# Kernel tuning notes

Measured on AMD Instinct MI355X. Metric: run time of the kernel, lower is better.

## Reference

```python
import jax, jax.numpy as jnp
import numpy as np

SPATIAL_SHAPES = ((64, 64), (32, 32), (16, 16), (8, 8))  # (H_l, W_l) per level
N_HEADS, N_LEVELS, N_POINTS = 8, 4, 4
EMBED, HEAD_DIM = 256, 32


def _bilinear_sample(v_lvl, loc, H, W):
    """grid_sample(mode=bilinear, padding=zeros, align_corners=False).

    v_lvl: (B, nH, H*W, d)   loc: (B, Nq, nH, P, 2) with (x, y) in [0, 1].
    Returns (B, nH, Nq, P, d).
    """
    B, nH, _, d = v_lvl.shape
    Nq, P = loc.shape[1], loc.shape[3]
    g = 2.0 * loc - 1.0                      # normalized [-1, 1]
    px = ((g[..., 0] + 1.0) * W - 1.0) * 0.5  # pixel coords, align_corners=False
    py = ((g[..., 1] + 1.0) * H - 1.0) * 0.5
    x0 = jnp.floor(px); y0 = jnp.floor(py)
    wx = px - x0; wy = py - y0
    x0i = x0.astype(jnp.int32); y0i = y0.astype(jnp.int32)
    acc = jnp.zeros((B, nH, Nq * P, d), v_lvl.dtype)
    corners = ((0, 0, (1 - wx) * (1 - wy)), (1, 0, wx * (1 - wy)),
               (0, 1, (1 - wx) * wy), (1, 1, wx * wy))
    for dx, dy, w in corners:
        xi = x0i + dx; yi = y0i + dy
        valid = (xi >= 0) & (xi < W) & (yi >= 0) & (yi < H)
        idx = jnp.clip(yi, 0, H - 1) * W + jnp.clip(xi, 0, W - 1)  # (B,Nq,nH,P)
        idx_t = idx.transpose(0, 2, 1, 3).reshape(B, nH, Nq * P)
        wm = jnp.where(valid, w, 0.0).astype(v_lvl.dtype)
        wm = wm.transpose(0, 2, 1, 3).reshape(B, nH, Nq * P, 1)
        gathered = jnp.take_along_axis(v_lvl, idx_t[..., None], axis=2)
        acc = acc + wm * gathered
    return acc.reshape(B, nH, Nq, P, d)


def setup_inputs() -> dict:
    key = jax.random.key(0)
    ks = jax.random.split(key, 12)
    B, Nq = 4, sum(H * W for H, W in SPATIAL_SHAPES)
    Nv = Nq
    s = 1.0 / np.sqrt(EMBED)
    return {
        "query": jax.random.normal(ks[0], (B, Nq, EMBED), jnp.float32),
        "value": jax.random.normal(ks[1], (B, Nv, EMBED), jnp.float32),
        "reference_points": jax.random.uniform(ks[2], (B, Nq, N_LEVELS, 2), jnp.float32),
        "value_proj_w": jax.random.normal(ks[3], (EMBED, EMBED), jnp.float32) * s,
        "value_proj_b": jnp.zeros((EMBED,), jnp.float32),
        "offsets_w": jax.random.normal(ks[4], (EMBED, N_HEADS * N_LEVELS * N_POINTS * 2), jnp.float32) * (0.05 * s),
        "offsets_b": jax.random.normal(ks[5], (N_HEADS * N_LEVELS * N_POINTS * 2,), jnp.float32) * 2.0,
        "attn_w_w": jax.random.normal(ks[6], (EMBED, N_HEADS * N_LEVELS * N_POINTS), jnp.float32) * s,
        "attn_w_b": jnp.zeros((N_HEADS * N_LEVELS * N_POINTS,), jnp.float32),
        "out_w": jax.random.normal(ks[7], (EMBED, EMBED), jnp.float32) * s,
        "out_b": jnp.zeros((EMBED,), jnp.float32),
    }


def reference(query, value, reference_points, value_proj_w, value_proj_b,
              offsets_w, offsets_b, attn_w_w, attn_w_b, out_w, out_b):
    B, Nq, C = query.shape
    Nv = value.shape[1]
    v = (value @ value_proj_w + value_proj_b).reshape(B, Nv, N_HEADS, HEAD_DIM)
    off = (query @ offsets_w + offsets_b).reshape(B, Nq, N_HEADS, N_LEVELS, N_POINTS, 2)
    aw = (query @ attn_w_w + attn_w_b).reshape(B, Nq, N_HEADS, N_LEVELS * N_POINTS)
    aw = jax.nn.softmax(aw, axis=-1).reshape(B, Nq, N_HEADS, N_LEVELS, N_POINTS)
    norm = jnp.array([[W, H] for H, W in SPATIAL_SHAPES], dtype=query.dtype)  # (L,2) as (W,H)
    loc = reference_points[:, :, None, :, None, :] + off / norm[None, None, None, :, None, :]
    out = jnp.zeros((B, Nq, N_HEADS, HEAD_DIM), query.dtype)
    cursor = 0
    for l, (H, W) in enumerate(SPATIAL_SHAPES):
        v_lvl = v[:, cursor:cursor + H * W].transpose(0, 2, 1, 3)  # (B,nH,HW,d)
        cursor += H * W
        sampled = _bilinear_sample(v_lvl, loc[:, :, :, l], H, W)   # (B,nH,Nq,P,d)
        out = out + jnp.einsum('bnhp,bhnpd->bnhd', aw[:, :, :, l], sampled)
    return out.reshape(B, Nq, C) @ out_w + out_b
```

## Files before the change

kernel.cpp:

```cpp
#include <hip/hip_runtime.h>
#include <hip/hip_bf16.h>
#include <math.h>

#define B_ 4
#define NQ 5440
#define M_ROWS (B_ * NQ)
#define NH 8
#define NL 4
#define NP 4
#define HD 32

typedef __attribute__((ext_vector_type(8))) short bf16x8;
typedef __attribute__((ext_vector_type(4))) short bf16x4;
typedef __attribute__((ext_vector_type(4))) float f32x4;
typedef _Float16 f16;

static __device__ __forceinline__ unsigned short f2bf(float f) {
  union { float f; unsigned u; } v; v.f = f;
  unsigned r = (v.u + 0x7fffu + ((v.u >> 16) & 1u)) >> 16;
  return (unsigned short)r;
}
static __device__ __forceinline__ float bits2f(unsigned u) {
  union { unsigned u; float f; } v; v.u = u; return v.f;
}

__global__ __launch_bounds__(256) void prep_all(
    const float* __restrict__ value, const float* __restrict__ query,
    unsigned short* __restrict__ value_bf, unsigned short* __restrict__ query_bf,
    const float* __restrict__ vpw, const float* __restrict__ offw,
    const float* __restrict__ attnw, const float* __restrict__ outw,
    const float* __restrict__ offb, const float* __restrict__ attnb,
    unsigned short* __restrict__ vp_t, unsigned short* __restrict__ q_t,
    unsigned short* __restrict__ out_t, float* __restrict__ biasq, int n4) {
  int id = blockIdx.x * 256 + threadIdx.x;
  if (id < 2 * n4) {
    const float* src; unsigned short* dst; int j;
    if (id < n4) { src = value; dst = value_bf; j = id; }
    else { src = query; dst = query_bf; j = id - n4; }
    float4 f = ((const float4*)src)[j];
    bf16x4 o;
    o[0] = (short)f2bf(f.x); o[1] = (short)f2bf(f.y);
    o[2] = (short)f2bf(f.z); o[3] = (short)f2bf(f.w);
    ((bf16x4*)dst)[j] = o;
    return;
  }
  int w = id - 2 * n4;
  if (w < 65536) {
    int n = w >> 8, k = w & 255;
    vp_t[w] = f2bf(vpw[k * 256 + n]);
  } else if (w < 163840) {
    int q = w - 65536; int n = q >> 8, k = q & 255;
    q_t[q] = f2bf(n < 256 ? offw[k * 256 + n] : attnw[k * 128 + (n - 256)]);
  } else if (w < 229376) {
    int o = w - 163840; int n = o >> 8, k = o & 255;
    out_t[o] = f2bf(outw[k * 256 + n]);
  } else if (w < 229760) {
    int j = w - 229376;
    biasq[j] = j < 256 ? offb[j] : attnb[j - 256];
  }
}

__global__ __launch_bounds__(256) void gemm12_kernel(
    const unsigned short* __restrict__ valbf, const unsigned short* __restrict__ qrybf,
    const unsigned short* __restrict__ wt_vp, const unsigned short* __restrict__ wt_q,
    const float* __restrict__ vp_b, const float* __restrict__ biasq,
    unsigned short* __restrict__ v_bf, f16* __restrict__ offaw_h) {
  __shared__ unsigned short Bs[8 * 64 * 32];
  const int t = threadIdx.x;
  const int lane = t & 63, wid = t >> 6;
  const int qd = lane >> 4, l16 = lane & 15;
  const int g = blockIdx.x;
  const int grp = g / 80, r = g % 80;
  int by, bx;
  if (grp < 21) { by = grp * 8 + (r & 7); bx = r >> 3; }
  else          { by = 168 + (r & 1);     bx = r >> 1; }
  const int bm = by * 128;
  const bool isv = bx < 4;
  const int bn = isv ? bx * 64 : (bx - 4) * 64;
  const unsigned short* A  = isv ? valbf : qrybf;
  const unsigned short* Wt = isv ? wt_vp : wt_q;

  const unsigned short* bg = Wt + (size_t)(bn + (t >> 2)) * 256 + (t & 3) * 8;
  unsigned short* bs_b = Bs + (t & 192) * 8;
#pragma unroll
  for (int j = 0; j < 8; ++j)
    __builtin_amdgcn_global_load_lds(
        (const __attribute__((address_space(1))) void*)(bg + j * 32),
        (__attribute__((address_space(3))) void*)(bs_b + j * 2048), 16, 0, 0);

  const unsigned short* ar0 = A + (size_t)(bm + wid * 32 + l16) * 256 + qd * 8;
  const unsigned short* ar1 = ar0 + 16 * 256;
  __syncthreads();

  f32x4 acc[2][4] = {};
#pragma unroll
  for (int j = 0; j < 8; ++j) {
    const bf16x8 af0 = *(const bf16x8*)(ar0 + j * 32);
    const bf16x8 af1 = *(const bf16x8*)(ar1 + j * 32);
    const unsigned short* bt = Bs + j * 2048 + l16 * 32 + qd * 8;
#pragma unroll
    for (int ni = 0; ni < 4; ++ni) {
      const bf16x8 bf = *(const bf16x8*)(bt + ni * 512);
      acc[0][ni] = __builtin_amdgcn_mfma_f32_16x16x32_bf16(af0, bf, acc[0][ni], 0, 0, 0);
      acc[1][ni] = __builtin_amdgcn_mfma_f32_16x16x32_bf16(af1, bf, acc[1][ni], 0, 0, 0);
    }
  }
  if (isv) {
#pragma unroll
    for (int ni = 0; ni < 4; ++ni) {
      const int c = bn + ni * 16 + l16;
      const float bb = vp_b[c];
      const int h = c >> 5, d = c & 31;
#pragma unroll
      for (int mi = 0; mi < 2; ++mi)
#pragma unroll
        for (int rr = 0; rr < 4; ++rr) {
          const int gm = bm + wid * 32 + mi * 16 + qd * 4 + rr;
          const int b = gm / NQ, pix = gm - b * NQ;
          v_bf[((size_t)(b * NH + h) * NQ + pix) * HD + d] = f2bf(acc[mi][ni][rr] + bb);
        }
    }
  } else {
#pragma unroll
    for (int ni = 0; ni < 4; ++ni) {
      const int c = bn + ni * 16 + l16;
      const float bb = biasq[c];
#pragma unroll
      for (int mi = 0; mi < 2; ++mi)
#pragma unroll
        for (int rr = 0; rr < 4; ++rr) {
          const int gm = bm + wid * 32 + mi * 16 + qd * 4 + rr;
          offaw_h[(size_t)gm * 384 + c] = (f16)(acc[mi][ni][rr] + bb);
        }
    }
  }
}

__global__ __launch_bounds__(256) void gemm_out_kernel(
    const unsigned short* __restrict__ attn_bf, const unsigned short* __restrict__ wt_out,
    const float* __restrict__ out_b, float* __restrict__ out) {
  __shared__ unsigned short Bs[8 * 64 * 32];
  const int t = threadIdx.x;
  const int lane = t & 63, wid = t >> 6;
  const int qd = lane >> 4, l16 = lane & 15;
  const int g = blockIdx.x;
  const int grp = g / 32, r = g % 32;
  int by, bx;
  if (grp < 21) { by = grp * 8 + (r & 7); bx = r >> 3; }
  else          { by = 168 + (r & 1);     bx = r >> 1; }
  const int bm = by * 128, bn = bx * 64;

  const unsigned short* bg = wt_out + (size_t)(bn + (t >> 2)) * 256 + (t & 3) * 8;
  unsigned short* bs_b = Bs + (t & 192) * 8;
#pragma unroll
  for (int j = 0; j < 8; ++j)
    __builtin_amdgcn_global_load_lds(
        (const __attribute__((address_space(1))) void*)(bg + j * 32),
        (__attribute__((address_space(3))) void*)(bs_b + j * 2048), 16, 0, 0);

  const unsigned short* ar0 = attn_bf + (size_t)(bm + wid * 32 + l16) * 256 + qd * 8;
  const unsigned short* ar1 = ar0 + 16 * 256;
  __syncthreads();

  f32x4 acc[2][4] = {};
#pragma unroll
  for (int j = 0; j < 8; ++j) {
    const bf16x8 af0 = *(const bf16x8*)(ar0 + j * 32);
    const bf16x8 af1 = *(const bf16x8*)(ar1 + j * 32);
    const unsigned short* bt = Bs + j * 2048 + l16 * 32 + qd * 8;
#pragma unroll
    for (int ni = 0; ni < 4; ++ni) {
      const bf16x8 bf = *(const bf16x8*)(bt + ni * 512);
      acc[0][ni] = __builtin_amdgcn_mfma_f32_16x16x32_bf16(af0, bf, acc[0][ni], 0, 0, 0);
      acc[1][ni] = __builtin_amdgcn_mfma_f32_16x16x32_bf16(af1, bf, acc[1][ni], 0, 0, 0);
    }
  }
#pragma unroll
  for (int ni = 0; ni < 4; ++ni) {
    const int c = bn + ni * 16 + l16;
    const float bb = out_b[c];
#pragma unroll
    for (int mi = 0; mi < 2; ++mi)
#pragma unroll
      for (int rr = 0; rr < 4; ++rr) {
        const int gm = bm + wid * 32 + mi * 16 + qd * 4 + rr;
        out[(size_t)gm * 256 + c] = acc[mi][ni][rr] + bb;
      }
  }
}

__global__ __launch_bounds__(256) void sample_fused_kernel(
    const unsigned short* __restrict__ v, const float* __restrict__ refp,
    const f16* __restrict__ offaw_h, unsigned short* __restrict__ out) {
  __shared__ float s_off[8 * 384];
  __shared__ float s_ref[64];
  __shared__ unsigned s_offs[16 * 64 * 4];
  __shared__ float s_wts[16 * 64 * 4];
  const int t = threadIdx.x;
  const int blk = blockIdx.x;
  const int b = (blk & 7) >> 1;
  const int q0loc = ((blk >> 3) * 2 + (blk & 1)) * 8;
  const int q0 = b * NQ + q0loc;

  {
    const unsigned* src = (const unsigned*)(offaw_h + (size_t)q0 * 384);
#pragma unroll
    for (int i = 0; i < 6; ++i) {
      const int idx = t + i * 256;
      union { unsigned u; f16 h[2]; } cv; cv.u = src[idx];
      s_off[2 * idx]     = (float)cv.h[0];
      s_off[2 * idx + 1] = (float)cv.h[1];
    }
    if (t < 64) s_ref[t] = refp[(size_t)q0 * 8 + t];
  }
  __syncthreads();
  if (t < 64) {
    float* p = s_off + (t >> 3) * 384 + 256 + (t & 7) * 16;
    float m = -1e30f;
#pragma unroll
    for (int j = 0; j < 16; ++j) m = fmaxf(m, p[j]);
    float e[16]; float s = 0.f;
#pragma unroll
    for (int j = 0; j < 16; ++j) { e[j] = __expf(p[j] - m); s += e[j]; }
    const float inv = 1.f / s;
#pragma unroll
    for (int j = 0; j < 16; ++j) p[j] = e[j] * inv;
  }
  __syncthreads();
  {
    const int qh = t & 63, q = qh >> 3, h = qh & 7, l = t >> 6;
    const int HS[NL]      = {64, 32, 16, 8};
    const int LVL_OFF[NL] = {0, 4096, 5120, 5376};
    const int H = HS[l], W = HS[l];
    const float rx = s_ref[q * 8 + l * 2 + 0];
    const float ry = s_ref[q * 8 + l * 2 + 1];
    const unsigned vbase = (unsigned)(((b * NH + h) * NQ + LVL_OFF[l]) * 64);
#pragma unroll
    for (int pp = 0; pp < 4; ++pp) {
      const int p = l * 4 + pp;
      const float ox = s_off[q * 384 + h * 32 + l * 8 + pp * 2 + 0];
      const float oy = s_off[q * 384 + h * 32 + l * 8 + pp * 2 + 1];
      const float a  = s_off[q * 384 + 256 + h * 16 + p];
      const float px = rx * (float)W + ox - 0.5f;
      const float py = ry * (float)H + oy - 0.5f;
      const float x0f = floorf(px), y0f = floorf(py);
      const int x0 = (int)x0f, y0 = (int)y0f;
      const int x1 = x0 + 1, y1 = y0 + 1;
      const float wx = px - x0f, wy = py - y0f;
      const float m_x0 = (x0 >= 0 && x0 < W) ? 1.f : 0.f;
      const float m_x1 = (x1 >= 0 && x1 < W) ? 1.f : 0.f;
      const float m_y0 = (y0 >= 0 && y0 < H) ? 1.f : 0.f;
      const float m_y1 = (y1 >= 0 && y1 < H) ? 1.f : 0.f;
      const int cx0 = min(max(x0, 0), W - 1), cx1 = min(max(x1, 0), W - 1);
      const int cy0 = min(max(y0, 0), H - 1), cy1 = min(max(y1, 0), H - 1);
      const int ti = (p * 64 + qh) * 4;
      uint4 o4;
      o4.x = vbase + (unsigned)((cy0 * W + cx0) * 64);
      o4.y = vbase + (unsigned)((cy0 * W + cx1) * 64);
      o4.z = vbase + (unsigned)((cy1 * W + cx0) * 64);
      o4.w = vbase + (unsigned)((cy1 * W + cx1) * 64);
      float4 w4;
      w4.x = a * (1.f - wx) * (1.f - wy) * m_x0 * m_y0;
      w4.y = a * wx * (1.f - wy) * m_x1 * m_y0;
      w4.z = a * (1.f - wx) * wy * m_x0 * m_y1;
      w4.w = a * wx * wy * m_x1 * m_y1;
      *(uint4*)&s_offs[ti] = o4;
      *(float4*)&s_wts[ti] = w4;
    }
  }
  __syncthreads();
  const int lane = t & 63, wave = t >> 6;
  const int qloc = wave * 2 + (lane >> 5);
  const int h = (lane >> 2) & 7, d8 = lane & 3;
  const int tqh = qloc * 8 + h;
  const char* vB = (const char*)v;
  const int dof = d8 * 16;
  float acc[8] = {};
#pragma unroll 4
  for (int p = 0; p < 16; ++p) {
    const uint4  o4 = *(const uint4*)&s_offs[(p * 64 + tqh) * 4];
    const float4 w4 = *(const float4*)&s_wts[(p * 64 + tqh) * 4];
    const unsigned off[4] = {o4.x, o4.y, o4.z, o4.w};
    const float wt[4] = {w4.x, w4.y, w4.z, w4.w};
#pragma unroll
    for (int c = 0; c < 4; ++c) {
      union { bf16x8 v8; unsigned u[4]; } cc;
      cc.v8 = *(const bf16x8*)(vB + off[c] + dof);
      const float w = wt[c];
#pragma unroll
      for (int k = 0; k < 4; ++k) {
        acc[2 * k]     += w * bits2f(cc.u[k] << 16);
        acc[2 * k + 1] += w * bits2f(cc.u[k] & 0xffff0000u);
      }
    }
  }
  const int bq = q0 + qloc;
  bf16x8 ov;
#pragma unroll
  for (int k = 0; k < 8; ++k) ov[k] = (short)f2bf(acc[k]);
  *(bf16x8*)(out + (size_t)bq * 256 + h * HD + d8 * 8) = ov;
}

extern "C" void kernel_launch(void* const* d_in, const int* in_sizes, int n_in,
                              void* d_out, int out_size, void* d_ws, size_t ws_size,
                              hipStream_t stream) {
  const float* query        = (const float*)d_in[0];
  const float* value        = (const float*)d_in[1];
  const float* refp         = (const float*)d_in[2];
  const float* value_proj_w = (const float*)d_in[3];
  const float* value_proj_b = (const float*)d_in[4];
  const float* offsets_w    = (const float*)d_in[5];
  const float* offsets_b    = (const float*)d_in[6];
  const float* attn_w_w     = (const float*)d_in[7];
  const float* attn_w_b     = (const float*)d_in[8];
  const float* out_w        = (const float*)d_in[9];
  const float* out_b        = (const float*)d_in[10];
  float* out = (float*)d_out;

  const int M = M_ROWS;
  const size_t SZ_V   = (size_t)M * 256 * 2;
  const size_t SZ_OFF = (size_t)M * 384 * 2;
  char* w = (char*)d_ws;
  unsigned short* value_bf = (unsigned short*)w;
  unsigned short* attn_bf  = (unsigned short*)w;
  unsigned short* query_bf = (unsigned short*)(w + SZ_V);
  unsigned short* v_bf     = (unsigned short*)(w + 2 * SZ_V);
  f16* offaw_h             = (f16*)(w + 3 * SZ_V);
  char* wts                = w + 3 * SZ_V + SZ_OFF;
  unsigned short* wt_vp    = (unsigned short*)wts;
  unsigned short* wt_q     = wt_vp + 65536;
  unsigned short* wt_out   = wt_q + 98304;
  float* biasq             = (float*)(wt_out + 65536);

  dim3 blk(256);
  const int n4 = M * 64;
  const int prep_blocks = (2 * n4 + 229760 + 255) / 256;
  prep_all<<<prep_blocks, blk, 0, stream>>>(
      value, query, value_bf, query_bf,
      value_proj_w, offsets_w, attn_w_w, out_w, offsets_b, attn_w_b,
      wt_vp, wt_q, wt_out, biasq, n4);
  gemm12_kernel<<<1700, blk, 0, stream>>>(
      value_bf, query_bf, wt_vp, wt_q, value_proj_b, biasq, v_bf, offaw_h);
  sample_fused_kernel<<<M / 8, blk, 0, stream>>>(v_bf, refp, offaw_h, attn_bf);
  gemm_out_kernel<<<680, blk, 0, stream>>>(attn_bf, wt_out, out_b, out);
}
```

Measured before the change: 174.1 us.

## Shrink sampler LDS with padded aliased layout, fp16 weights, packed FMA

The sampling kernel's shared memory is rearranged. Offsets and attention logits go into padded rows to avoid bank conflicts, and the per-tap offset table aliases the same buffer after values are pulled into registers behind an extra barrier. Bilinear corner weights are stored as fp16 instead of fp32, and accumulation uses two-wide float vectors so the compiler can emit packed FMA. The aim is a much smaller LDS footprint for higher occupancy and fewer ALU instructions in the gather loop, at the cost of an extra sync and reduced weight precision.

Result: slower. 184.5 us (+5.9%).

```diff
diff --git a/kernel.cpp b/kernel.cpp
--- a/kernel.cpp
+++ b/kernel.cpp
@@ -13,7 +13,9 @@
 typedef __attribute__((ext_vector_type(8))) short bf16x8;
 typedef __attribute__((ext_vector_type(4))) short bf16x4;
 typedef __attribute__((ext_vector_type(4))) float f32x4;
+typedef __attribute__((ext_vector_type(2))) float f32x2;
 typedef _Float16 f16;
+typedef __attribute__((ext_vector_type(4))) _Float16 f16x4;
 
 static __device__ __forceinline__ unsigned short f2bf(float f) {
   union { float f; unsigned u; } v; v.f = f;
@@ -192,10 +194,13 @@
 __global__ __launch_bounds__(256) void sample_fused_kernel(
     const unsigned short* __restrict__ v, const float* __restrict__ refp,
     const f16* __restrict__ offaw_h, unsigned short* __restrict__ out) {
-  __shared__ float s_off[8 * 384];
-  __shared__ float s_ref[64];
-  __shared__ unsigned s_offs[16 * 64 * 4];
-  __shared__ float s_wts[16 * 64 * 4];
+  __shared__ __align__(16) char smem[24832];
+  float*    s_offp = (float*)smem;
+  float*    s_aw   = (float*)(smem + 8448);
+  unsigned* s_toff = (unsigned*)smem;
+  f16*      s_twt  = (f16*)(smem + 16384);
+  float*    s_ref  = (float*)(smem + 24576);
+
   const int t = threadIdx.x;
   const int blk = blockIdx.x;
   const int b = (blk & 7) >> 1;
@@ -207,15 +212,24 @@
 #pragma unroll
     for (int i = 0; i < 6; ++i) {
       const int idx = t + i * 256;
+      const int q = idx / 192, u = idx - q * 192;
       union { unsigned u; f16 h[2]; } cv; cv.u = src[idx];
-      s_off[2 * idx]     = (float)cv.h[0];
-      s_off[2 * idx + 1] = (float)cv.h[1];
+      const float lo = (float)cv.h[0], hi = (float)cv.h[1];
+      const int c = 2 * u;
+      if (c < 256) {
+        float* d = s_offp + (q * 8 + (c >> 5)) * 33 + (c & 31);
+        d[0] = lo; d[1] = hi;
+      } else {
+        const int cc = c - 256;
+        float* d = s_aw + (q * 8 + (cc >> 4)) * 17 + (cc & 15);
+        d[0] = lo; d[1] = hi;
+      }
     }
     if (t < 64) s_ref[t] = refp[(size_t)q0 * 8 + t];
   }
   __syncthreads();
   if (t < 64) {
-    float* p = s_off + (t >> 3) * 384 + 256 + (t & 7) * 16;
+    float* p = s_aw + t * 17;
     float m = -1e30f;
 #pragma unroll
     for (int j = 0; j < 16; ++j) m = fmaxf(m, p[j]);
@@ -227,20 +241,27 @@
     for (int j = 0; j < 16; ++j) p[j] = e[j] * inv;
   }
   __syncthreads();
+  const int qh = t & 63, l = t >> 6;
+  const int q = qh >> 3, h = qh & 7;
+  float offv[8], awv[4];
+#pragma unroll
+  for (int i = 0; i < 8; ++i) offv[i] = s_offp[qh * 33 + l * 8 + i];
+#pragma unroll
+  for (int i = 0; i < 4; ++i) awv[i] = s_aw[qh * 17 + l * 4 + i];
+  const float rx = s_ref[q * 8 + l * 2 + 0];
+  const float ry = s_ref[q * 8 + l * 2 + 1];
+  __syncthreads();
   {
-    const int qh = t & 63, q = qh >> 3, h = qh & 7, l = t >> 6;
     const int HS[NL]      = {64, 32, 16, 8};
     const int LVL_OFF[NL] = {0, 4096, 5120, 5376};
     const int H = HS[l], W = HS[l];
-    const float rx = s_ref[q * 8 + l * 2 + 0];
-    const float ry = s_ref[q * 8 + l * 2 + 1];
     const unsigned vbase = (unsigned)(((b * NH + h) * NQ + LVL_OFF[l]) * 64);
 #pragma unroll
     for (int pp = 0; pp < 4; ++pp) {
       const int p = l * 4 + pp;
-      const float ox = s_off[q * 384 + h * 32 + l * 8 + pp * 2 + 0];
-      const float oy = s_off[q * 384 + h * 32 + l * 8 + pp * 2 + 1];
-      const float a  = s_off[q * 384 + 256 + h * 16 + p];
+      const float ox = offv[pp * 2 + 0];
+      const float oy = offv[pp * 2 + 1];
+      const float a  = awv[pp];
       const float px = rx * (float)W + ox - 0.5f;
       const float py = ry * (float)H + oy - 0.5f;
       const float x0f = floorf(px), y0f = floorf(py);
@@ -259,46 +280,49 @@
       o4.y = vbase + (unsigned)((cy0 * W + cx1) * 64);
       o4.z = vbase + (unsigned)((cy1 * W + cx0) * 64);
       o4.w = vbase + (unsigned)((cy1 * W + cx1) * 64);
-      float4 w4;
-      w4.x = a * (1.f - wx) * (1.f - wy) * m_x0 * m_y0;
-      w4.y = a * wx * (1.f - wy) * m_x1 * m_y0;
-      w4.z = a * (1.f - wx) * wy * m_x0 * m_y1;
-      w4.w = a * wx * wy * m_x1 * m_y1;
-      *(uint4*)&s_offs[ti] = o4;
-      *(float4*)&s_wts[ti] = w4;
+      f16x4 w4;
+      w4[0] = (f16)(a * (1.f - wx) * (1.f - wy) * m_x0 * m_y0);
+      w4[1] = (f16)(a * wx * (1.f - wy) * m_x1 * m_y0);
+      w4[2] = (f16)(a * (1.f - wx) * wy * m_x0 * m_y1);
+      w4[3] = (f16)(a * wx * wy * m_x1 * m_y1);
+      *(uint4*)&s_toff[ti] = o4;
+      *(f16x4*)&s_twt[ti] = w4;
     }
   }
   __syncthreads();
   const int lane = t & 63, wave = t >> 6;
   const int qloc = wave * 2 + (lane >> 5);
-  const int h = (lane >> 2) & 7, d8 = lane & 3;
-  const int tqh = qloc * 8 + h;
+  const int gh = (lane >> 2) & 7, d8 = lane & 3;
+  const int tqh = qloc * 8 + gh;
   const char* vB = (const char*)v;
   const int dof = d8 * 16;
-  float acc[8] = {};
+  f32x2 acc2[4] = {};
 #pragma unroll 4
   for (int p = 0; p < 16; ++p) {
-    const uint4  o4 = *(const uint4*)&s_offs[(p * 64 + tqh) * 4];
-    const float4 w4 = *(const float4*)&s_wts[(p * 64 + tqh) * 4];
+    const uint4 o4 = *(const uint4*)&s_toff[(p * 64 + tqh) * 4];
+    const f16x4 wh = *(const f16x4*)&s_twt[(p * 64 + tqh) * 4];
     const unsigned off[4] = {o4.x, o4.y, o4.z, o4.w};
-    const float wt[4] = {w4.x, w4.y, w4.z, w4.w};
+    const float wt[4] = {(float)wh[0], (float)wh[1], (float)wh[2], (float)wh[3]};
 #pragma unroll
     for (int c = 0; c < 4; ++c) {
       union { bf16x8 v8; unsigned u[4]; } cc;
       cc.v8 = *(const bf16x8*)(vB + off[c] + dof);
-      const float w = wt[c];
+      const f32x2 w2 = {wt[c], wt[c]};
 #pragma unroll
       for (int k = 0; k < 4; ++k) {
-        acc[2 * k]     += w * bits2f(cc.u[k] << 16);
-        acc[2 * k + 1] += w * bits2f(cc.u[k] & 0xffff0000u);
+        const f32x2 val = {bits2f(cc.u[k] << 16), bits2f(cc.u[k] & 0xffff0000u)};
+        acc2[k] += w2 * val;
       }
     }
   }
   const int bq = q0 + qloc;
   bf16x8 ov;
 #pragma unroll
-  for (int k = 0; k < 8; ++k) ov[k] = (short)f2bf(acc[k]);
-  *(bf16x8*)(out + (size_t)bq * 256 + h * HD + d8 * 8) = ov;
+  for (int k = 0; k < 4; ++k) {
+    ov[2 * k]     = (short)f2bf(acc2[k][0]);
+    ov[2 * k + 1] = (short)f2bf(acc2[k][1]);
+  }
+  *(bf16x8*)(out + (size_t)bq * 256 + gh * HD + d8 * 8) = ov;
 }
 
 extern "C" void kernel_launch(void* const* d_in, const int* in_sizes, int n_in,
```
